# Performance work log

Measured on AMD Instinct MI355X. Metric: run time of the kernel, lower is better.

## Reference

```python
import jax, jax.numpy as jnp
import numpy as np

H = 64
NP_, PD = 100000, 1024
NS_, SD = 50000, 512
EP, ES, EL = 3200000, 1600000, 2000000


def gcn_conv(x, ei, W, b):
    """PyG GCNConv: add self-loops, symmetric deg^-1/2 normalization, linear, scatter-add, bias."""
    N = x.shape[0]
    loop = jnp.arange(N, dtype=ei.dtype)
    src = jnp.concatenate([ei[0], loop])
    dst = jnp.concatenate([ei[1], loop])
    deg = jax.ops.segment_sum(jnp.ones_like(src, dtype=x.dtype), dst, num_segments=N)
    dinv = jax.lax.rsqrt(deg)  # deg >= 1 thanks to self-loops
    norm = (dinv[src] * dinv[dst])[:, None]  # [E+N, 1]
    h = x @ W  # [N, H]
    out = jax.ops.segment_sum(h[src] * norm, dst, num_segments=N)
    return out + b


def setup_inputs() -> dict:
    key = jax.random.key(0)
    ks = jax.random.split(key, 16)
    w = lambda k, s: jax.random.normal(k, s, dtype=jnp.float32) * 0.02
    z = lambda s: jnp.zeros(s, dtype=jnp.float32)
    return {
        "x_protein": jax.random.normal(ks[0], (NP_, PD), dtype=jnp.float32),
        "x_substrate": jax.random.normal(ks[1], (NS_, SD), dtype=jnp.float32),
        "ei_protein": jax.random.randint(ks[2], (2, EP), 0, NP_, dtype=jnp.int64),
        "ei_substrate": jax.random.randint(ks[3], (2, ES), 0, NS_, dtype=jnp.int64),
        "edges_protein": jax.random.randint(ks[4], (EL,), 0, NP_, dtype=jnp.int64),
        "edges_substrate": jax.random.randint(ks[5], (EL,), 0, NS_, dtype=jnp.int64),
        "Wp1": w(ks[6], (PD, H)), "bp1": z((H,)),
        "Ws1": w(ks[7], (SD, H)), "bs1": z((H,)),
        "Wp2": w(ks[8], (H, H)), "bp2": z((H,)),
        "Ws2": w(ks[9], (H, H)), "bs2": z((H,)),
        "Wproj": w(ks[10], (2 * H, 2 * H)), "bproj": z((2 * H,)),
        "Wl1": w(ks[11], (2 * H, H)), "bl1": z((H,)),
        "Wl2": w(ks[12], (H, 1)), "bl2": z((1,)),
    }


def reference(x_protein, x_substrate, ei_protein, ei_substrate,
              edges_protein, edges_substrate,
              Wp1, bp1, Ws1, bs1, Wp2, bp2, Ws2, bs2,
              Wproj, bproj, Wl1, bl1, Wl2, bl2):
    # encode (no activation between convs, matching the source)
    z_protein = gcn_conv(gcn_conv(x_protein, ei_protein, Wp1, bp1), ei_protein, Wp2, bp2)
    z_substrate = gcn_conv(gcn_conv(x_substrate, ei_substrate, Ws1, bs1), ei_substrate, Ws2, bs2)
    # gather endpoints, concat, project, MLP link predictor
    z_combined = jnp.concatenate([z_protein[edges_protein], z_substrate[edges_substrate]], axis=-1)  # [EL, 2H]
    z_projected = z_combined @ Wproj + bproj
    h = jax.nn.relu(z_projected @ Wl1 + bl1)
    return (h @ Wl2 + bl2).squeeze()  # [EL]
```

## Files before the change

kernel.cpp:

```cpp
#include <hip/hip_runtime.h>

#define NPn 100000
#define NSn 50000
#define PDk 1024
#define SDk 512
#define EPe 3200000
#define ESe 1600000
#define ELe 2000000
#define NB_P 196
#define NB_S 98
#define CHUNK 8192

__global__ void k_bhist(const int* __restrict__ dst, int E, int* __restrict__ bcnt,
                        int NB) {
  __shared__ int h[256];
  int t = threadIdx.x;
  if (t < NB) h[t] = 0;
  __syncthreads();
  for (int i = blockIdx.x * 256 + t; i < E; i += gridDim.x * 256)
    atomicAdd(&h[dst[i] >> 9], 1);
  __syncthreads();
  if (t < NB && h[t]) atomicAdd(&bcnt[t], h[t]);
}

__global__ void k_bscan(const int* __restrict__ bcnt, int* __restrict__ boff,
                        int* __restrict__ bcur, int NB, int E, int* __restrict__ row,
                        int N) {
  __shared__ int wsum[4];
  int t = threadIdx.x, lane = t & 63, w = t >> 6;
  int v = (t < NB) ? bcnt[t] : 0;
  int x = v;
#pragma unroll
  for (int off = 1; off < 64; off <<= 1) {
    int y = __shfl_up(x, off);
    if (lane >= off) x += y;
  }
  if (lane == 63) wsum[w] = x;
  __syncthreads();
  int woff = 0;
  for (int j = 0; j < w; ++j) woff += wsum[j];
  int ex = woff + x - v;
  if (t < NB) { boff[t] = ex; bcur[t] = ex; }
  if (t == 0) { boff[NB] = E; row[N] = E; }
}

__global__ __launch_bounds__(256) void k_bucket2(const int* __restrict__ src,
                                                 const int* __restrict__ dst, int E,
                                                 int* __restrict__ bcur,
                                                 int* __restrict__ bdata, int NB) {
  __shared__ int hist[256];
  __shared__ int lofs[256];
  __shared__ int delta[256];
  __shared__ int lcur[256];
  __shared__ int wsum[4];
  __shared__ int stage[CHUNK];
  int t = threadIdx.x;
  int base = blockIdx.x * CHUNK;
  int cnt = min(CHUNK, E - base);
  hist[t] = 0;
  __syncthreads();
  for (int i = t; i < cnt; i += 256) atomicAdd(&hist[dst[base + i] >> 9], 1);
  __syncthreads();
  int v = hist[t];
  int lane = t & 63, w = t >> 6;
  int x = v;
#pragma unroll
  for (int off = 1; off < 64; off <<= 1) {
    int y = __shfl_up(x, off);
    if (lane >= off) x += y;
  }
  if (lane == 63) wsum[w] = x;
  __syncthreads();
  int woff = 0;
  for (int j = 0; j < w; ++j) woff += wsum[j];
  int ex = woff + x - v;
  lofs[t] = ex;
  lcur[t] = ex;
  if (t < NB) delta[t] = atomicAdd(&bcur[t], v) - ex;
  __syncthreads();
  for (int i = t; i < cnt; i += 256) {
    int d = dst[base + i];
    int b = d >> 9;
    int p = atomicAdd(&lcur[b], 1);
    stage[p] = (src[base + i] << 9) | (d & 511);
  }
  __syncthreads();
  for (int i = t; i < cnt; i += 256) {
    int lo = 0, hi = NB;
    while (hi - lo > 1) {
      int mid = (lo + hi) >> 1;
      if (lofs[mid] <= i) lo = mid; else hi = mid;
    }
    bdata[delta[lo] + i] = stage[i];
  }
}

__global__ __launch_bounds__(256) void k_build(const int* __restrict__ bdata,
                                               const int* __restrict__ boff,
                                               int* __restrict__ col,
                                               int* __restrict__ row,
                                               float* __restrict__ dinv, int N) {
  __shared__ int hist[512];
  __shared__ int excl[512];
  __shared__ int wsum[4];
  int b = blockIdx.x, t = threadIdx.x;
  int s = boff[b], e = boff[b + 1];
  int n0 = b << 9;
  hist[t] = 0; hist[t + 256] = 0;
  __syncthreads();
  for (int i = s + t; i < e; i += 256) atomicAdd(&hist[bdata[i] & 511], 1);
  __syncthreads();
  int a0 = hist[2 * t], a1 = hist[2 * t + 1];
  int ps = a0 + a1;
  int lane = t & 63, w = t >> 6;
  int x = ps;
#pragma unroll
  for (int off = 1; off < 64; off <<= 1) {
    int y = __shfl_up(x, off);
    if (lane >= off) x += y;
  }
  if (lane == 63) wsum[w] = x;
  __syncthreads();
  int woff = 0;
  for (int j = 0; j < w; ++j) woff += wsum[j];
  int ex = woff + x - ps;
  excl[2 * t] = ex;
  excl[2 * t + 1] = ex + a0;
  __syncthreads();
  for (int l = t; l < 512; l += 256) {
    int n = n0 + l;
    if (n < N) {
      row[n] = s + excl[l];
      dinv[n] = rsqrtf((float)(hist[l] + 1));
    }
  }
  __syncthreads();
  for (int i = s + t; i < e; i += 256) {
    int v = bdata[i];
    int p = atomicAdd(&excl[v & 511], 1);
    col[s + p] = v >> 9;
  }
}

__global__ __launch_bounds__(256) void k_gemm128(const float* __restrict__ A,
                                                 const float* __restrict__ W,
                                                 float* __restrict__ C, int M, int K) {
  __shared__ float as[32][132];
  __shared__ float bs[32][68];
  int tid = threadIdx.x;
  int tx = tid & 15;
  int ty = tid >> 4;
  int row0 = blockIdx.x * 128;
  float acc[8][4] = {};
  for (int k0 = 0; k0 < K; k0 += 32) {
    {
      int r = tid >> 1;
      int kk = (tid & 1) * 16;
      int grow = row0 + r;
      float4 v0 = make_float4(0.f, 0.f, 0.f, 0.f), v1 = v0, v2 = v0, v3 = v0;
      if (grow < M) {
        const float* srcp = A + (size_t)grow * K + k0 + kk;
        v0 = ((const float4*)srcp)[0];
        v1 = ((const float4*)srcp)[1];
        v2 = ((const float4*)srcp)[2];
        v3 = ((const float4*)srcp)[3];
      }
      as[kk + 0][r] = v0.x;  as[kk + 1][r] = v0.y;  as[kk + 2][r] = v0.z;  as[kk + 3][r] = v0.w;
      as[kk + 4][r] = v1.x;  as[kk + 5][r] = v1.y;  as[kk + 6][r] = v1.z;  as[kk + 7][r] = v1.w;
      as[kk + 8][r] = v2.x;  as[kk + 9][r] = v2.y;  as[kk + 10][r] = v2.z; as[kk + 11][r] = v2.w;
      as[kk + 12][r] = v3.x; as[kk + 13][r] = v3.y; as[kk + 14][r] = v3.z; as[kk + 15][r] = v3.w;
    }
    {
      int kk = tid >> 3;
      int n = (tid & 7) * 8;
      const float* srcp = W + (size_t)(k0 + kk) * 64 + n;
      float4 v0 = *(const float4*)(srcp);
      float4 v1 = *(const float4*)(srcp + 4);
      *(float4*)&bs[kk][n] = v0;
      *(float4*)&bs[kk][n + 4] = v1;
    }
    __syncthreads();
#pragma unroll
    for (int kk = 0; kk < 32; ++kk) {
      float4 a0 = *(const float4*)&as[kk][ty * 8];
      float4 a1 = *(const float4*)&as[kk][ty * 8 + 4];
      float4 b = *(const float4*)&bs[kk][tx * 4];
      float av[8] = {a0.x, a0.y, a0.z, a0.w, a1.x, a1.y, a1.z, a1.w};
      float bv[4] = {b.x, b.y, b.z, b.w};
#pragma unroll
      for (int i = 0; i < 8; ++i)
#pragma unroll
        for (int j = 0; j < 4; ++j) acc[i][j] += av[i] * bv[j];
    }
    __syncthreads();
  }
  int r0 = row0 + ty * 8, c0 = tx * 4;
#pragma unroll
  for (int i = 0; i < 8; ++i) {
    int r = r0 + i;
    if (r < M)
      *(float4*)&C[(size_t)r * 64 + c0] =
          make_float4(acc[i][0], acc[i][1], acc[i][2], acc[i][3]);
  }
}

__global__ __launch_bounds__(256) void k_agg(const float* __restrict__ h,
                                             const int* __restrict__ row,
                                             const int* __restrict__ col,
                                             const float* __restrict__ dinv,
                                             const float* __restrict__ bias,
                                             float* __restrict__ out, int N) {
  int w = threadIdx.x >> 6, lane = threadIdx.x & 63;
  int g = lane >> 4;
  int f = lane & 15;
  int i = blockIdx.x * 4 + w;
  if (i >= N) return;
  float di = dinv[i];
  int s = row[i], e = row[i + 1];
  float4 acc = make_float4(0.f, 0.f, 0.f, 0.f);
  if (g == 0) {
    float4 hv = *(const float4*)&h[(size_t)i * 64 + f * 4];
    acc.x = di * hv.x; acc.y = di * hv.y; acc.z = di * hv.z; acc.w = di * hv.w;
  }
  for (int base = s; base < e; base += 64) {
    int idx = base + lane;
    int cidx = (idx < e) ? col[idx] : 0;
    float dv = (idx < e) ? dinv[cidx] : 0.f;
    int cnt = min(64, e - base);
    int nt = (cnt + 3) >> 2;
    for (int t = 0; t < nt; ++t) {
      int sl = t * 4 + g;
      int j = __shfl(cidx, sl);
      float dj = __shfl(dv, sl);
      float4 hv = *(const float4*)&h[(size_t)j * 64 + f * 4];
      acc.x += dj * hv.x; acc.y += dj * hv.y; acc.z += dj * hv.z; acc.w += dj * hv.w;
    }
  }
  acc.x += __shfl_xor(acc.x, 16); acc.y += __shfl_xor(acc.y, 16);
  acc.z += __shfl_xor(acc.z, 16); acc.w += __shfl_xor(acc.w, 16);
  acc.x += __shfl_xor(acc.x, 32); acc.y += __shfl_xor(acc.y, 32);
  acc.z += __shfl_xor(acc.z, 32); acc.w += __shfl_xor(acc.w, 32);
  if (lane < 16) {
    float4 b4 = *(const float4*)&bias[f * 4];
    float4 o;
    o.x = di * acc.x + b4.x; o.y = di * acc.y + b4.y;
    o.z = di * acc.z + b4.z; o.w = di * acc.w + b4.w;
    *(float4*)&out[(size_t)i * 64 + f * 4] = o;
  }
}

__global__ __launch_bounds__(1024) void k_fold2(
    const float* __restrict__ Wproj, const float* __restrict__ bproj,
    const float* __restrict__ Wl1, const float* __restrict__ bl1,
    const float* __restrict__ Wp2, const float* __restrict__ bp2,
    const float* __restrict__ Ws2, const float* __restrict__ bs2,
    float* __restrict__ W2m_p, float* __restrict__ c2_p, float* __restrict__ W2m_s,
    float* __restrict__ c2_s, float* __restrict__ cvec) {
  int which = blockIdx.x;
  const float* W2 = which ? Ws2 : Wp2;
  const float* b2v = which ? bs2 : bp2;
  float* W2m = which ? W2m_s : W2m_p;
  float* c2 = which ? c2_s : c2_p;
  __shared__ float M[64][64];
  int t = threadIdx.x;
  for (int idx = t; idx < 4096; idx += 1024) {
    int a = idx >> 6, c = idx & 63;
    const float* wr = Wproj + (size_t)(which * 64 + a) * 128;
    float sum = 0.f;
    for (int k = 0; k < 128; ++k) sum += wr[k] * Wl1[(size_t)k * 64 + c];
    M[a][c] = sum;
  }
  __syncthreads();
  for (int idx = t; idx < 4096; idx += 1024) {
    int a = idx >> 6, c = idx & 63;
    float sum = 0.f;
    for (int k = 0; k < 64; ++k) sum += W2[a * 64 + k] * M[k][c];
    W2m[idx] = sum;
  }
  if (t < 64) {
    float sum = 0.f;
    for (int k = 0; k < 64; ++k) sum += b2v[k] * M[k][t];
    c2[t] = sum;
  }
  if (which == 0 && t >= 64 && t < 128) {
    int c = t - 64;
    float sum = bl1[c];
    for (int k = 0; k < 128; ++k) sum += bproj[k] * Wl1[(size_t)k * 64 + c];
    cvec[c] = sum;
  }
}

__global__ void k_link(const float* __restrict__ P, const float* __restrict__ S,
                       const int* __restrict__ ep, const int* __restrict__ es,
                       const float* __restrict__ cvec, const float* __restrict__ wl2,
                       const float* __restrict__ bl2, float* __restrict__ out, int EL) {
  int lane = threadIdx.x & 63;
  int g = lane >> 4;
  int f = lane & 15;
  int wave = threadIdx.x >> 6;
  float4 c4 = *(const float4*)&cvec[f * 4];
  float4 w4 = *(const float4*)&wl2[f * 4];
  float b2 = bl2[0];
  int e0 = blockIdx.x * 16 + wave * 4 + g;
  int step = gridDim.x * 16;
  for (int e = e0; e < EL; e += step) {
    int rp = ep[e], rs = es[e];
    float4 p4 = *(const float4*)&P[(size_t)rp * 64 + f * 4];
    float4 s4 = *(const float4*)&S[(size_t)rs * 64 + f * 4];
    float u, acc;
    u = p4.x + s4.x + c4.x; acc  = fmaxf(u, 0.f) * w4.x;
    u = p4.y + s4.y + c4.y; acc += fmaxf(u, 0.f) * w4.y;
    u = p4.z + s4.z + c4.z; acc += fmaxf(u, 0.f) * w4.z;
    u = p4.w + s4.w + c4.w; acc += fmaxf(u, 0.f) * w4.w;
    acc += __shfl_xor(acc, 1);
    acc += __shfl_xor(acc, 2);
    acc += __shfl_xor(acc, 4);
    acc += __shfl_xor(acc, 8);
    if (f == 0) out[e] = acc + b2;
  }
}

extern "C" void kernel_launch(void* const* d_in, const int* in_sizes, int n_in,
                              void* d_out, int out_size, void* d_ws, size_t ws_size,
                              hipStream_t stream) {
  const float* x_p  = (const float*)d_in[0];
  const float* x_s  = (const float*)d_in[1];
  const int*   ei_p = (const int*)d_in[2];
  const int*   ei_s = (const int*)d_in[3];
  const int*   ed_p = (const int*)d_in[4];
  const int*   ed_s = (const int*)d_in[5];
  const float* Wp1 = (const float*)d_in[6];  const float* bp1 = (const float*)d_in[7];
  const float* Ws1 = (const float*)d_in[8];  const float* bs1 = (const float*)d_in[9];
  const float* Wp2 = (const float*)d_in[10]; const float* bp2 = (const float*)d_in[11];
  const float* Ws2 = (const float*)d_in[12]; const float* bs2 = (const float*)d_in[13];
  const float* Wproj = (const float*)d_in[14]; const float* bproj = (const float*)d_in[15];
  const float* Wl1 = (const float*)d_in[16]; const float* bl1 = (const float*)d_in[17];
  const float* Wl2 = (const float*)d_in[18]; const float* bl2 = (const float*)d_in[19];
  float* out = (float*)d_out;

  char* wsp = (char*)d_ws;
  size_t off = 0;
  auto alloc = [&](size_t b) -> void* {
    void* p = wsp + off;
    off = (off + b + 255) & ~(size_t)255;
    return p;
  };
  float* bufA_p = (float*)alloc((size_t)NPn * 64 * 4);
  float* bufB_p = (float*)alloc((size_t)NPn * 64 * 4);
  float* bufA_s = (float*)alloc((size_t)NSn * 64 * 4);
  float* bufB_s = (float*)alloc((size_t)NSn * 64 * 4);
  int*   col_p  = (int*)alloc((size_t)EPe * 4);
  int*   col_s  = (int*)alloc((size_t)ESe * 4);
  float* dinv_p = (float*)alloc((size_t)NPn * 4);
  float* dinv_s = (float*)alloc((size_t)NSn * 4);
  int*   row_p  = (int*)alloc((size_t)(NPn + 1) * 4);
  int*   row_s  = (int*)alloc((size_t)(NSn + 1) * 4);
  int*   bcnt_p = (int*)alloc(256 * 4);
  int*   bcnt_s = (int*)alloc(256 * 4);
  int*   boff_p = (int*)alloc(257 * 4);
  int*   boff_s = (int*)alloc(257 * 4);
  int*   bcur_p = (int*)alloc(256 * 4);
  int*   bcur_s = (int*)alloc(256 * 4);
  float* W2m_p  = (float*)alloc(64 * 64 * 4);
  float* W2m_s  = (float*)alloc(64 * 64 * 4);
  float* c2_p   = (float*)alloc(64 * 4);
  float* c2_s   = (float*)alloc(64 * 4);
  float* cvec   = (float*)alloc(64 * 4);
  (void)ws_size; (void)n_in; (void)in_sizes; (void)out_size;

  int* bdata_p = (int*)bufA_p;
  int* bdata_s = (int*)bufA_s;

  const int* src_p = ei_p;           const int* dst_p = ei_p + EPe;
  const int* src_s = ei_s;           const int* dst_s = ei_s + ESe;

  hipMemsetAsync(bcnt_p, 0, 256 * 4, stream);
  hipMemsetAsync(bcnt_s, 0, 256 * 4, stream);

  k_fold2<<<2, 1024, 0, stream>>>(Wproj, bproj, Wl1, bl1, Wp2, bp2, Ws2, bs2,
                                  W2m_p, c2_p, W2m_s, c2_s, cvec);

  k_bhist<<<1280, 256, 0, stream>>>(dst_p, EPe, bcnt_p, NB_P);
  k_bhist<<<1280, 256, 0, stream>>>(dst_s, ESe, bcnt_s, NB_S);
  k_bscan<<<1, 256, 0, stream>>>(bcnt_p, boff_p, bcur_p, NB_P, EPe, row_p, NPn);
  k_bscan<<<1, 256, 0, stream>>>(bcnt_s, boff_s, bcur_s, NB_S, ESe, row_s, NSn);
  k_bucket2<<<(EPe + CHUNK - 1) / CHUNK, 256, 0, stream>>>(src_p, dst_p, EPe, bcur_p,
                                                           bdata_p, NB_P);
  k_bucket2<<<(ESe + CHUNK - 1) / CHUNK, 256, 0, stream>>>(src_s, dst_s, ESe, bcur_s,
                                                           bdata_s, NB_S);
  k_build<<<NB_P, 256, 0, stream>>>(bdata_p, boff_p, col_p, row_p, dinv_p, NPn);
  k_build<<<NB_S, 256, 0, stream>>>(bdata_s, boff_s, col_s, row_s, dinv_s, NSn);

  k_gemm128<<<(NPn + 127) / 128, 256, 0, stream>>>(x_p, Wp1, bufA_p, NPn, PDk);
  k_agg<<<(NPn + 3) / 4, 256, 0, stream>>>(bufA_p, row_p, col_p, dinv_p, bp1, bufB_p, NPn);
  k_gemm128<<<(NPn + 127) / 128, 256, 0, stream>>>(bufB_p, W2m_p, bufA_p, NPn, 64);
  k_agg<<<(NPn + 3) / 4, 256, 0, stream>>>(bufA_p, row_p, col_p, dinv_p, c2_p, bufB_p, NPn);

  k_gemm128<<<(NSn + 127) / 128, 256, 0, stream>>>(x_s, Ws1, bufA_s, NSn, SDk);
  k_agg<<<(NSn + 3) / 4, 256, 0, stream>>>(bufA_s, row_s, col_s, dinv_s, bs1, bufB_s, NSn);
  k_gemm128<<<(NSn + 127) / 128, 256, 0, stream>>>(bufB_s, W2m_s, bufA_s, NSn, 64);
  k_agg<<<(NSn + 3) / 4, 256, 0, stream>>>(bufA_s, row_s, col_s, dinv_s, c2_s, bufB_s, NSn);

  k_link<<<(ELe + 15) / 16, 256, 0, stream>>>(bufB_p, bufB_s, ed_p, ed_s, cvec, Wl2,
                                              bl2, out, ELe);
}
```

Before: 1.583 ms.

## Store intermediate node features as bf16 to halve gather traffic

Intermediate 64-wide node feature buffers are now stored as bf16 instead of fp32. The GEMM writes bf16, aggregation and link kernels read bf16 and accumulate in fp32, and the wave layout changes to 8 lanes per row with 8 rows per wave step. Because the bf16 buffers are smaller, the bucket scratch gets its own allocation instead of aliasing bufA. The goal is to halve the bytes moved by the random-gather kernels (aggregation and link), at the cost of bf16 rounding error in outputs.

```diff
diff --git a/kernel.cpp b/kernel.cpp
--- a/kernel.cpp
+++ b/kernel.cpp
@@ -10,6 +10,16 @@
 #define NB_P 196
 #define NB_S 98
 #define CHUNK 8192
+
+__device__ __forceinline__ float blo(unsigned u) { return __uint_as_float(u << 16); }
+__device__ __forceinline__ float bhi(unsigned u) { return __uint_as_float(u & 0xFFFF0000u); }
+__device__ __forceinline__ unsigned f2b(float x) {
+  unsigned u = __float_as_uint(x);
+  return (u + 0x7FFFu + ((u >> 16) & 1u)) >> 16;
+}
+__device__ __forceinline__ unsigned pack2(float a, float b) {
+  return f2b(a) | (f2b(b) << 16);
+}
 
 __global__ void k_bhist(const int* __restrict__ dst, int E, int* __restrict__ bcnt,
                         int NB) {
@@ -142,9 +152,11 @@
   }
 }
 
-__global__ __launch_bounds__(256) void k_gemm128(const float* __restrict__ A,
+template <int ABF>
+__global__ __launch_bounds__(256) void k_gemm128(const void* __restrict__ Av,
                                                  const float* __restrict__ W,
-                                                 float* __restrict__ C, int M, int K) {
+                                                 unsigned short* __restrict__ C,
+                                                 int M, int K) {
   __shared__ float as[32][132];
   __shared__ float bs[32][68];
   int tid = threadIdx.x;
@@ -157,18 +169,35 @@
       int r = tid >> 1;
       int kk = (tid & 1) * 16;
       int grow = row0 + r;
-      float4 v0 = make_float4(0.f, 0.f, 0.f, 0.f), v1 = v0, v2 = v0, v3 = v0;
-      if (grow < M) {
-        const float* srcp = A + (size_t)grow * K + k0 + kk;
-        v0 = ((const float4*)srcp)[0];
-        v1 = ((const float4*)srcp)[1];
-        v2 = ((const float4*)srcp)[2];
-        v3 = ((const float4*)srcp)[3];
+      if (ABF) {
+        uint4 u0 = make_uint4(0, 0, 0, 0), u1 = u0;
+        if (grow < M) {
+          const uint4* p =
+              (const uint4*)((const unsigned short*)Av + (size_t)grow * K + k0 + kk);
+          u0 = p[0]; u1 = p[1];
+        }
+        as[kk + 0][r] = blo(u0.x);  as[kk + 1][r] = bhi(u0.x);
+        as[kk + 2][r] = blo(u0.y);  as[kk + 3][r] = bhi(u0.y);
+        as[kk + 4][r] = blo(u0.z);  as[kk + 5][r] = bhi(u0.z);
+        as[kk + 6][r] = blo(u0.w);  as[kk + 7][r] = bhi(u0.w);
+        as[kk + 8][r] = blo(u1.x);  as[kk + 9][r] = bhi(u1.x);
+        as[kk + 10][r] = blo(u1.y); as[kk + 11][r] = bhi(u1.y);
+        as[kk + 12][r] = blo(u1.z); as[kk + 13][r] = bhi(u1.z);
+        as[kk + 14][r] = blo(u1.w); as[kk + 15][r] = bhi(u1.w);
+      } else {
+        float4 v0 = make_float4(0.f, 0.f, 0.f, 0.f), v1 = v0, v2 = v0, v3 = v0;
+        if (grow < M) {
+          const float* srcp = (const float*)Av + (size_t)grow * K + k0 + kk;
+          v0 = ((const float4*)srcp)[0];
+          v1 = ((const float4*)srcp)[1];
+          v2 = ((const float4*)srcp)[2];
+          v3 = ((const float4*)srcp)[3];
+        }
+        as[kk + 0][r] = v0.x;  as[kk + 1][r] = v0.y;  as[kk + 2][r] = v0.z;  as[kk + 3][r] = v0.w;
+        as[kk + 4][r] = v1.x;  as[kk + 5][r] = v1.y;  as[kk + 6][r] = v1.z;  as[kk + 7][r] = v1.w;
+        as[kk + 8][r] = v2.x;  as[kk + 9][r] = v2.y;  as[kk + 10][r] = v2.z; as[kk + 11][r] = v2.w;
+        as[kk + 12][r] = v3.x; as[kk + 13][r] = v3.y; as[kk + 14][r] = v3.z; as[kk + 15][r] = v3.w;
       }
-      as[kk + 0][r] = v0.x;  as[kk + 1][r] = v0.y;  as[kk + 2][r] = v0.z;  as[kk + 3][r] = v0.w;
-      as[kk + 4][r] = v1.x;  as[kk + 5][r] = v1.y;  as[kk + 6][r] = v1.z;  as[kk + 7][r] = v1.w;
-      as[kk + 8][r] = v2.x;  as[kk + 9][r] = v2.y;  as[kk + 10][r] = v2.z; as[kk + 11][r] = v2.w;
-      as[kk + 12][r] = v3.x; as[kk + 13][r] = v3.y; as[kk + 14][r] = v3.z; as[kk + 15][r] = v3.w;
     }
     {
       int kk = tid >> 3;
@@ -198,54 +227,69 @@
 #pragma unroll
   for (int i = 0; i < 8; ++i) {
     int r = r0 + i;
-    if (r < M)
-      *(float4*)&C[(size_t)r * 64 + c0] =
-          make_float4(acc[i][0], acc[i][1], acc[i][2], acc[i][3]);
-  }
-}
-
-__global__ __launch_bounds__(256) void k_agg(const float* __restrict__ h,
+    if (r < M) {
+      uint2 o;
+      o.x = pack2(acc[i][0], acc[i][1]);
+      o.y = pack2(acc[i][2], acc[i][3]);
+      *(uint2*)&C[(size_t)r * 64 + c0] = o;
+    }
+  }
+}
+
+__global__ __launch_bounds__(256) void k_agg(const unsigned short* __restrict__ h,
                                              const int* __restrict__ row,
                                              const int* __restrict__ col,
                                              const float* __restrict__ dinv,
                                              const float* __restrict__ bias,
-                                             float* __restrict__ out, int N) {
+                                             unsigned short* __restrict__ out, int N) {
   int w = threadIdx.x >> 6, lane = threadIdx.x & 63;
-  int g = lane >> 4;
-  int f = lane & 15;
+  int g = lane >> 3;
+  int f = lane & 7;
   int i = blockIdx.x * 4 + w;
   if (i >= N) return;
   float di = dinv[i];
   int s = row[i], e = row[i + 1];
-  float4 acc = make_float4(0.f, 0.f, 0.f, 0.f);
+  float4 aA = make_float4(0.f, 0.f, 0.f, 0.f), aB = aA;
   if (g == 0) {
-    float4 hv = *(const float4*)&h[(size_t)i * 64 + f * 4];
-    acc.x = di * hv.x; acc.y = di * hv.y; acc.z = di * hv.z; acc.w = di * hv.w;
+    uint4 hv = ((const uint4*)(h + (size_t)i * 64))[f];
+    aA.x = di * blo(hv.x); aA.y = di * bhi(hv.x);
+    aA.z = di * blo(hv.y); aA.w = di * bhi(hv.y);
+    aB.x = di * blo(hv.z); aB.y = di * bhi(hv.z);
+    aB.z = di * blo(hv.w); aB.w = di * bhi(hv.w);
   }
   for (int base = s; base < e; base += 64) {
     int idx = base + lane;
     int cidx = (idx < e) ? col[idx] : 0;
     float dv = (idx < e) ? dinv[cidx] : 0.f;
     int cnt = min(64, e - base);
-    int nt = (cnt + 3) >> 2;
+    int nt = (cnt + 7) >> 3;
     for (int t = 0; t < nt; ++t) {
-      int sl = t * 4 + g;
+      int sl = t * 8 + g;
       int j = __shfl(cidx, sl);
       float dj = __shfl(dv, sl);
-      float4 hv = *(const float4*)&h[(size_t)j * 64 + f * 4];
-      acc.x += dj * hv.x; acc.y += dj * hv.y; acc.z += dj * hv.z; acc.w += dj * hv.w;
-    }
-  }
-  acc.x += __shfl_xor(acc.x, 16); acc.y += __shfl_xor(acc.y, 16);
-  acc.z += __shfl_xor(acc.z, 16); acc.w += __shfl_xor(acc.w, 16);
-  acc.x += __shfl_xor(acc.x, 32); acc.y += __shfl_xor(acc.y, 32);
-  acc.z += __shfl_xor(acc.z, 32); acc.w += __shfl_xor(acc.w, 32);
-  if (lane < 16) {
-    float4 b4 = *(const float4*)&bias[f * 4];
-    float4 o;
-    o.x = di * acc.x + b4.x; o.y = di * acc.y + b4.y;
-    o.z = di * acc.z + b4.z; o.w = di * acc.w + b4.w;
-    *(float4*)&out[(size_t)i * 64 + f * 4] = o;
+      uint4 hv = ((const uint4*)(h + (size_t)j * 64))[f];
+      aA.x += dj * blo(hv.x); aA.y += dj * bhi(hv.x);
+      aA.z += dj * blo(hv.y); aA.w += dj * bhi(hv.y);
+      aB.x += dj * blo(hv.z); aB.y += dj * bhi(hv.z);
+      aB.z += dj * blo(hv.w); aB.w += dj * bhi(hv.w);
+    }
+  }
+#pragma unroll
+  for (int m = 8; m < 64; m <<= 1) {
+    aA.x += __shfl_xor(aA.x, m); aA.y += __shfl_xor(aA.y, m);
+    aA.z += __shfl_xor(aA.z, m); aA.w += __shfl_xor(aA.w, m);
+    aB.x += __shfl_xor(aB.x, m); aB.y += __shfl_xor(aB.y, m);
+    aB.z += __shfl_xor(aB.z, m); aB.w += __shfl_xor(aB.w, m);
+  }
+  if (lane < 8) {
+    float4 b0 = *(const float4*)&bias[f * 8];
+    float4 b1 = *(const float4*)&bias[f * 8 + 4];
+    uint4 o;
+    o.x = pack2(di * aA.x + b0.x, di * aA.y + b0.y);
+    o.y = pack2(di * aA.z + b0.z, di * aA.w + b0.w);
+    o.z = pack2(di * aB.x + b1.x, di * aB.y + b1.y);
+    o.w = pack2(di * aB.z + b1.z, di * aB.w + b1.w);
+    ((uint4*)(out + (size_t)i * 64))[f] = o;
   }
 }
 
@@ -290,32 +334,38 @@
   }
 }
 
-__global__ void k_link(const float* __restrict__ P, const float* __restrict__ S,
+__global__ void k_link(const unsigned short* __restrict__ P,
+                       const unsigned short* __restrict__ S,
                        const int* __restrict__ ep, const int* __restrict__ es,
                        const float* __restrict__ cvec, const float* __restrict__ wl2,
                        const float* __restrict__ bl2, float* __restrict__ out, int EL) {
   int lane = threadIdx.x & 63;
-  int g = lane >> 4;
-  int f = lane & 15;
+  int g = lane >> 3;
+  int f = lane & 7;
   int wave = threadIdx.x >> 6;
-  float4 c4 = *(const float4*)&cvec[f * 4];
-  float4 w4 = *(const float4*)&wl2[f * 4];
+  float4 c0 = *(const float4*)&cvec[f * 8];
+  float4 c1 = *(const float4*)&cvec[f * 8 + 4];
+  float4 w0 = *(const float4*)&wl2[f * 8];
+  float4 w1 = *(const float4*)&wl2[f * 8 + 4];
   float b2 = bl2[0];
-  int e0 = blockIdx.x * 16 + wave * 4 + g;
-  int step = gridDim.x * 16;
+  int e0 = blockIdx.x * 32 + wave * 8 + g;
+  int step = gridDim.x * 32;
   for (int e = e0; e < EL; e += step) {
     int rp = ep[e], rs = es[e];
-    float4 p4 = *(const float4*)&P[(size_t)rp * 64 + f * 4];
-    float4 s4 = *(const float4*)&S[(size_t)rs * 64 + f * 4];
+    uint4 pv = ((const uint4*)(P + (size_t)rp * 64))[f];
+    uint4 sv = ((const uint4*)(S + (size_t)rs * 64))[f];
     float u, acc;
-    u = p4.x + s4.x + c4.x; acc  = fmaxf(u, 0.f) * w4.x;
-    u = p4.y + s4.y + c4.y; acc += fmaxf(u, 0.f) * w4.y;
-    u = p4.z + s4.z + c4.z; acc += fmaxf(u, 0.f) * w4.z;
-    u = p4.w + s4.w + c4.w; acc += fmaxf(u, 0.f) * w4.w;
+    u = blo(pv.x) + blo(sv.x) + c0.x; acc  = fmaxf(u, 0.f) * w0.x;
+    u = bhi(pv.x) + bhi(sv.x) + c0.y; acc += fmaxf(u, 0.f) * w0.y;
+    u = blo(pv.y) + blo(sv.y) + c0.z; acc += fmaxf(u, 0.f) * w0.z;
+    u = bhi(pv.y) + bhi(sv.y) + c0.w; acc += fmaxf(u, 0.f) * w0.w;
+    u = blo(pv.z) + blo(sv.z) + c1.x; acc += fmaxf(u, 0.f) * w1.x;
+    u = bhi(pv.z) + bhi(sv.z) + c1.y; acc += fmaxf(u, 0.f) * w1.y;
+    u = blo(pv.w) + blo(sv.w) + c1.z; acc += fmaxf(u, 0.f) * w1.z;
+    u = bhi(pv.w) + bhi(sv.w) + c1.w; acc += fmaxf(u, 0.f) * w1.w;
     acc += __shfl_xor(acc, 1);
     acc += __shfl_xor(acc, 2);
     acc += __shfl_xor(acc, 4);
-    acc += __shfl_xor(acc, 8);
     if (f == 0) out[e] = acc + b2;
   }
 }
@@ -345,10 +395,10 @@
     off = (off + b + 255) & ~(size_t)255;
     return p;
   };
-  float* bufA_p = (float*)alloc((size_t)NPn * 64 * 4);
-  float* bufB_p = (float*)alloc((size_t)NPn * 64 * 4);
-  float* bufA_s = (float*)alloc((size_t)NSn * 64 * 4);
-  float* bufB_s = (float*)alloc((size_t)NSn * 64 * 4);
+  unsigned short* bufA_p = (unsigned short*)alloc((size_t)NPn * 64 * 2);
+  unsigned short* bufB_p = (unsigned short*)alloc((size_t)NPn * 64 * 2);
+  unsigned short* bufA_s = (unsigned short*)alloc((size_t)NSn * 64 * 2);
+  unsigned short* bufB_s = (unsigned short*)alloc((size_t)NSn * 64 * 2);
   int*   col_p  = (int*)alloc((size_t)EPe * 4);
   int*   col_s  = (int*)alloc((size_t)ESe * 4);
   float* dinv_p = (float*)alloc((size_t)NPn * 4);
@@ -366,10 +416,9 @@
   float* c2_p   = (float*)alloc(64 * 4);
   float* c2_s   = (float*)alloc(64 * 4);
   float* cvec   = (float*)alloc(64 * 4);
+  int* bdata_p = (int*)alloc((size_t)EPe * 4);
+  int* bdata_s = (int*)alloc((size_t)ESe * 4);
   (void)ws_size; (void)n_in; (void)in_sizes; (void)out_size;
-
-  int* bdata_p = (int*)bufA_p;
-  int* bdata_s = (int*)bufA_s;
 
   const int* src_p = ei_p;           const int* dst_p = ei_p + EPe;
   const int* src_s = ei_s;           const int* dst_s = ei_s + ESe;
@@ -391,16 +440,16 @@
   k_build<<<NB_P, 256, 0, stream>>>(bdata_p, boff_p, col_p, row_p, dinv_p, NPn);
   k_build<<<NB_S, 256, 0, stream>>>(bdata_s, boff_s, col_s, row_s, dinv_s, NSn);
 
-  k_gemm128<<<(NPn + 127) / 128, 256, 0, stream>>>(x_p, Wp1, bufA_p, NPn, PDk);
+  k_gemm128<0><<<(NPn + 127) / 128, 256, 0, stream>>>(x_p, Wp1, bufA_p, NPn, PDk);
   k_agg<<<(NPn + 3) / 4, 256, 0, stream>>>(bufA_p, row_p, col_p, dinv_p, bp1, bufB_p, NPn);
-  k_gemm128<<<(NPn + 127) / 128, 256, 0, stream>>>(bufB_p, W2m_p, bufA_p, NPn, 64);
+  k_gemm128<1><<<(NPn + 127) / 128, 256, 0, stream>>>(bufB_p, W2m_p, bufA_p, NPn, 64);
   k_agg<<<(NPn + 3) / 4, 256, 0, stream>>>(bufA_p, row_p, col_p, dinv_p, c2_p, bufB_p, NPn);
 
-  k_gemm128<<<(NSn + 127) / 128, 256, 0, stream>>>(x_s, Ws1, bufA_s, NSn, SDk);
+  k_gemm128<0><<<(NSn + 127) / 128, 256, 0, stream>>>(x_s, Ws1, bufA_s, NSn, SDk);
   k_agg<<<(NSn + 3) / 4, 256, 0, stream>>>(bufA_s, row_s, col_s, dinv_s, bs1, bufB_s, NSn);
-  k_gemm128<<<(NSn + 127) / 128, 256, 0, stream>>>(bufB_s, W2m_s, bufA_s, NSn, 64);
+  k_gemm128<1><<<(NSn + 127) / 128, 256, 0, stream>>>(bufB_s, W2m_s, bufA_s, NSn, 64);
   k_agg<<<(NSn + 3) / 4, 256, 0, stream>>>(bufA_s, row_s, col_s, dinv_s, c2_s, bufB_s, NSn);
 
-  k_link<<<(ELe + 15) / 16, 256, 0, stream>>>(bufB_p, bufB_s, ed_p, ed_s, cvec, Wl2,
+  k_link<<<(ELe + 31) / 32, 256, 0, stream>>>(bufB_p, bufB_s, ed_p, ed_s, cvec, Wl2,
                                               bl2, out, ELe);
 }
```

After: 1.403 ms. 1.13x faster.
